# Performance work log

Measured on AMD Instinct MI355X. Metric: run time of the kernel, lower is better.

## Reference

```python
import jax, jax.numpy as jnp
import numpy as np

NUM_SEGMENTS = 4480  # BATCH_SIZE * MAX_ATOMS = 64 * 70
ATOM_DIM = 64
BOND_DIM = 16
N_EDGES = 65536


def setup_inputs() -> dict:
    key = jax.random.key(0)
    k1, k2, k3, k4 = jax.random.split(key, 4)
    atom_feat = jax.random.normal(k1, (NUM_SEGMENTS, ATOM_DIM), dtype=jnp.float32)
    bond_feat = jax.random.normal(k2, (N_EDGES, BOND_DIM), dtype=jnp.float32)
    pair_idx = jax.random.randint(k3, (N_EDGES, 2), 0, NUM_SEGMENTS, dtype=jnp.int64)
    # glorot-uniform style kernel, zero bias (as in add_weight initializers)
    limit = float(np.sqrt(6.0 / (BOND_DIM + ATOM_DIM ** 2)))
    kernel = jax.random.uniform(k4, (BOND_DIM, ATOM_DIM ** 2), dtype=jnp.float32,
                                minval=-limit, maxval=limit)
    bias = jnp.zeros((ATOM_DIM ** 2,), dtype=jnp.float32)
    return {"atom_feat": atom_feat, "bond_feat": bond_feat,
            "pair_idx": pair_idx, "kernel": kernel, "bias": bias}


def reference(atom_feat, bond_feat, pair_idx, kernel, bias):
    atom_dim = atom_feat.shape[-1]
    # dense projection of bond features -> per-edge transform matrices
    bond_transformed = bond_feat @ kernel + bias               # [E, D*D]
    bond_transformed = bond_transformed.reshape(-1, atom_dim, atom_dim)  # [E, D, D]
    # gather neighbor (source) atom features per edge
    neighbor_feat = jnp.take(atom_feat, pair_idx[:, 1].astype(jnp.int32), axis=0)  # [E, D]
    # per-edge matrix-vector product
    messages = jnp.einsum('eij,ej->ei', bond_transformed, neighbor_feat)  # [E, D]
    # scatter-add into destination atoms
    return jax.ops.segment_sum(messages, pair_idx[:, 0].astype(jnp.int32),
                               num_segments=NUM_SEGMENTS)  # [NUM_SEGMENTS, D]
```

## Files before the change

kernel.cpp:

```cpp
#include <hip/hip_runtime.h>
#include <hip/hip_bf16.h>

#define NSEG   4480
#define ADIM   64
#define BDIM   16
#define NEDGE  65536
#define UPITCH 1088
#define LPITCH 68

__device__ __forceinline__ float bf2f(unsigned int bits_hi16) {
    union { unsigned int i; float f; } c; c.i = bits_hi16; return c.f;
}
__device__ __forceinline__ unsigned short f2bf(float f) {
    union { float f; unsigned int i; } c; c.f = f;
    unsigned int x = c.i;
    x += 0x7fffu + ((x >> 16) & 1u);
    return (unsigned short)(x >> 16);
}

__global__ __launch_bounds__(256) void proj_kernel(
    const float* __restrict__ atom,
    const float* __restrict__ kern,
    const float* __restrict__ bias,
    unsigned short* __restrict__ U,
    float* __restrict__ out)
{
    __shared__ float As[64 * LPITCH];
    __shared__ float Bs[64 * LPITCH];

    const int t      = threadIdx.x;
    const int bx     = blockIdx.x;
    const int by     = blockIdx.y;
    const int a_base = bx * 64;
    const int c_base = by * 64;

    {
        int gid = by * 70 * 256 + bx * 256 + t;
        if (gid < NSEG * ADIM / 4) {
            ((float4*)out)[gid] = make_float4(0.f, 0.f, 0.f, 0.f);
        }
    }

#pragma unroll
    for (int k = 0; k < 4; ++k) {
        int id  = t + k * 256;
        int row = id >> 4;
        int j0  = (id & 15) * 4;
        float4 v = *(const float4*)(atom + (size_t)(a_base + row) * ADIM + j0);
        As[(j0 + 0) * LPITCH + row] = v.x;
        As[(j0 + 1) * LPITCH + row] = v.y;
        As[(j0 + 2) * LPITCH + row] = v.z;
        As[(j0 + 3) * LPITCH + row] = v.w;
    }
#pragma unroll
    for (int k = 0; k < 4; ++k) {
        int id   = t + k * 256;
        int crow = id >> 4;
        int j0   = (id & 15) * 4;
        int c    = c_base + crow;
        const float* bsrc = (c < 1024)
            ? (kern + (size_t)(c & 15) * 4096 + (size_t)(c >> 4) * 64)
            : (bias + (size_t)(c - 1024) * 64);
        float4 v = *(const float4*)(bsrc + j0);
        Bs[(j0 + 0) * LPITCH + crow] = v.x;
        Bs[(j0 + 1) * LPITCH + crow] = v.y;
        Bs[(j0 + 2) * LPITCH + crow] = v.z;
        Bs[(j0 + 3) * LPITCH + crow] = v.w;
    }
    __syncthreads();

    const int tx = t & 15;
    const int ty = t >> 4;
    const int a0 = ty * 4;
    const int c0 = tx * 4;

    float acc[4][4] = {};
#pragma unroll 8
    for (int j = 0; j < 64; ++j) {
        float4 av = *(const float4*)(As + j * LPITCH + a0);
        float4 bv = *(const float4*)(Bs + j * LPITCH + c0);
        acc[0][0] = fmaf(av.x, bv.x, acc[0][0]);
        acc[0][1] = fmaf(av.x, bv.y, acc[0][1]);
        acc[0][2] = fmaf(av.x, bv.z, acc[0][2]);
        acc[0][3] = fmaf(av.x, bv.w, acc[0][3]);
        acc[1][0] = fmaf(av.y, bv.x, acc[1][0]);
        acc[1][1] = fmaf(av.y, bv.y, acc[1][1]);
        acc[1][2] = fmaf(av.y, bv.z, acc[1][2]);
        acc[1][3] = fmaf(av.y, bv.w, acc[1][3]);
        acc[2][0] = fmaf(av.z, bv.x, acc[2][0]);
        acc[2][1] = fmaf(av.z, bv.y, acc[2][1]);
        acc[2][2] = fmaf(av.z, bv.z, acc[2][2]);
        acc[2][3] = fmaf(av.z, bv.w, acc[2][3]);
        acc[3][0] = fmaf(av.w, bv.x, acc[3][0]);
        acc[3][1] = fmaf(av.w, bv.y, acc[3][1]);
        acc[3][2] = fmaf(av.w, bv.z, acc[3][2]);
        acc[3][3] = fmaf(av.w, bv.w, acc[3][3]);
    }

#pragma unroll
    for (int r = 0; r < 4; ++r) {
        ushort4 o;
        o.x = f2bf(acc[r][0]);
        o.y = f2bf(acc[r][1]);
        o.z = f2bf(acc[r][2]);
        o.w = f2bf(acc[r][3]);
        *(ushort4*)(U + (size_t)(a_base + a0 + r) * UPITCH + c_base + c0) = o;
    }
}

__global__ __launch_bounds__(256) void edge_kernel(
    const float*          __restrict__ bond,
    const int*            __restrict__ pair,
    const unsigned short* __restrict__ U,
    float*                __restrict__ out)
{
    const int t    = threadIdx.x;
    const int lane = t & 63;
    const int e    = blockIdx.x * 4 + (t >> 6);

    const int dst = pair[(size_t)e * 2 + 0];
    const int src = pair[(size_t)e * 2 + 1];

    const unsigned short* urow = U + (size_t)src * UPITCH;
    const uint4* up = (const uint4*)(urow + lane * 16);
    uint4 w0 = up[0];
    uint4 w1 = up[1];

    const float4* bp = (const float4*)(bond + (size_t)e * BDIM);
    float4 b0 = bp[0], b1 = bp[1], b2 = bp[2], b3 = bp[3];
    float b[16] = { b0.x, b0.y, b0.z, b0.w,  b1.x, b1.y, b1.z, b1.w,
                    b2.x, b2.y, b2.z, b2.w,  b3.x, b3.y, b3.z, b3.w };

    unsigned int w[8] = { w0.x, w0.y, w0.z, w0.w, w1.x, w1.y, w1.z, w1.w };

    float m = 0.f;
#pragma unroll
    for (int k = 0; k < 8; ++k) {
        float lo = bf2f(w[k] << 16);
        float hi = bf2f(w[k] & 0xffff0000u);
        m = fmaf(lo, b[2 * k],     m);
        m = fmaf(hi, b[2 * k + 1], m);
    }

    m += bf2f(((unsigned int)urow[1024 + lane]) << 16);

    atomicAdd(out + (size_t)dst * ADIM + lane, m);
}

extern "C" void kernel_launch(void* const* d_in, const int* in_sizes, int n_in,
                              void* d_out, int out_size, void* d_ws, size_t ws_size,
                              hipStream_t stream) {
    const float* atom = (const float*)d_in[0];
    const float* bond = (const float*)d_in[1];
    const int*   pair = (const int*)  d_in[2];
    const float* kern = (const float*)d_in[3];
    const float* bias = (const float*)d_in[4];

    float* out = (float*)d_out;
    unsigned short* U = (unsigned short*)d_ws;

    dim3 g1(NSEG / 64, UPITCH / 64);
    proj_kernel<<<g1, 256, 0, stream>>>(atom, kern, bias, U, out);

    edge_kernel<<<NEDGE / 4, 256, 0, stream>>>(bond, pair, U, out);
}
```

Baseline: 99.42 us.

## Bucket edges by source atom so each wave reuses one projected row

Adds a scatter kernel that groups edge ids by source atom into fixed-capacity slots, using atomic counters zeroed inside the projection kernel. The edge kernel now assigns two waves per source atom. Each wave loads that atom's bf16 transform row and bias term once and loops over its bucketed edges, instead of re-gathering the 2 KB row for every edge. This cuts redundant gather traffic. In exchange it adds a launch, an atomic bucketing pass, and a serial per-wave loop, and edges beyond the capacity of 96 per source would be silently dropped.

```diff
diff --git a/kernel.cpp b/kernel.cpp
--- a/kernel.cpp
+++ b/kernel.cpp
@@ -7,6 +7,7 @@
 #define NEDGE  65536
 #define UPITCH 1088
 #define LPITCH 68
+#define CAP    96
 
 __device__ __forceinline__ float bf2f(unsigned int bits_hi16) {
     union { unsigned int i; float f; } c; c.i = bits_hi16; return c.f;
@@ -23,7 +24,8 @@
     const float* __restrict__ kern,
     const float* __restrict__ bias,
     unsigned short* __restrict__ U,
-    float* __restrict__ out)
+    float* __restrict__ out,
+    int*   __restrict__ cnt)
 {
     __shared__ float As[64 * LPITCH];
     __shared__ float Bs[64 * LPITCH];
@@ -34,11 +36,12 @@
     const int a_base = bx * 64;
     const int c_base = by * 64;
 
-    {
-        int gid = by * 70 * 256 + bx * 256 + t;
-        if (gid < NSEG * ADIM / 4) {
-            ((float4*)out)[gid] = make_float4(0.f, 0.f, 0.f, 0.f);
-        }
+    if (by == 0) {
+        int gid = bx * 256 + t;
+        ((float4*)out)[gid] = make_float4(0.f, 0.f, 0.f, 0.f);
+    } else if (by == 1) {
+        int gid = bx * 256 + t;
+        if (gid < NSEG / 4) ((int4*)cnt)[gid] = make_int4(0, 0, 0, 0);
     }
 
 #pragma unroll
@@ -108,43 +111,60 @@
     }
 }
 
+__global__ __launch_bounds__(256) void scatter_kernel(
+    const int* __restrict__ pair, int* __restrict__ cnt, int* __restrict__ slot)
+{
+    int e   = blockIdx.x * 256 + threadIdx.x;
+    int src = pair[(size_t)e * 2 + 1];
+    int pos = atomicAdd(&cnt[src], 1);
+    if (pos < CAP) slot[src * CAP + pos] = e;
+}
+
 __global__ __launch_bounds__(256) void edge_kernel(
     const float*          __restrict__ bond,
     const int*            __restrict__ pair,
     const unsigned short* __restrict__ U,
+    const int*            __restrict__ cnt,
+    const int*            __restrict__ slot,
     float*                __restrict__ out)
 {
     const int t    = threadIdx.x;
     const int lane = t & 63;
-    const int e    = blockIdx.x * 4 + (t >> 6);
+    const int wid  = blockIdx.x * 4 + (t >> 6);
+    const int s    = wid >> 1;
+    const int half = wid & 1;
 
-    const int dst = pair[(size_t)e * 2 + 0];
-    const int src = pair[(size_t)e * 2 + 1];
-
-    const unsigned short* urow = U + (size_t)src * UPITCH;
+    const unsigned short* urow = U + (size_t)s * UPITCH;
     const uint4* up = (const uint4*)(urow + lane * 16);
     uint4 w0 = up[0];
     uint4 w1 = up[1];
+    unsigned int w[8] = { w0.x, w0.y, w0.z, w0.w, w1.x, w1.y, w1.z, w1.w };
+    float ub = bf2f(((unsigned int)urow[1024 + lane]) << 16);
 
-    const float4* bp = (const float4*)(bond + (size_t)e * BDIM);
-    float4 b0 = bp[0], b1 = bp[1], b2 = bp[2], b3 = bp[3];
-    float b[16] = { b0.x, b0.y, b0.z, b0.w,  b1.x, b1.y, b1.z, b1.w,
-                    b2.x, b2.y, b2.z, b2.w,  b3.x, b3.y, b3.z, b3.w };
+    int n = cnt[s];
+    if (n > CAP) n = CAP;
 
-    unsigned int w[8] = { w0.x, w0.y, w0.z, w0.w, w1.x, w1.y, w1.z, w1.w };
+    for (int k = half; k < n; k += 2) {
+        int e = slot[s * CAP + k];
+        e = __builtin_amdgcn_readfirstlane(e);
+        int dst = pair[(size_t)e * 2 + 0];
 
-    float m = 0.f;
+        const float4* bp = (const float4*)(bond + (size_t)e * BDIM);
+        float4 b0 = bp[0], b1 = bp[1], b2 = bp[2], b3 = bp[3];
+        float b[16] = { b0.x, b0.y, b0.z, b0.w,  b1.x, b1.y, b1.z, b1.w,
+                        b2.x, b2.y, b2.z, b2.w,  b3.x, b3.y, b3.z, b3.w };
+
+        float m = ub;
 #pragma unroll
-    for (int k = 0; k < 8; ++k) {
-        float lo = bf2f(w[k] << 16);
-        float hi = bf2f(w[k] & 0xffff0000u);
-        m = fmaf(lo, b[2 * k],     m);
-        m = fmaf(hi, b[2 * k + 1], m);
+        for (int q = 0; q < 8; ++q) {
+            float lo = bf2f(w[q] << 16);
+            float hi = bf2f(w[q] & 0xffff0000u);
+            m = fmaf(lo, b[2 * q],     m);
+            m = fmaf(hi, b[2 * q + 1], m);
+        }
+
+        atomicAdd(out + (size_t)dst * ADIM + lane, m);
     }
-
-    m += bf2f(((unsigned int)urow[1024 + lane]) << 16);
-
-    atomicAdd(out + (size_t)dst * ADIM + lane, m);
 }
 
 extern "C" void kernel_launch(void* const* d_in, const int* in_sizes, int n_in,
@@ -157,10 +177,16 @@
     const float* bias = (const float*)d_in[4];
 
     float* out = (float*)d_out;
-    unsigned short* U = (unsigned short*)d_ws;
+
+    char* ws = (char*)d_ws;
+    unsigned short* U = (unsigned short*)ws;
+    int* cnt  = (int*)(ws + (size_t)NSEG * UPITCH * 2);
+    int* slot = cnt + NSEG;
 
     dim3 g1(NSEG / 64, UPITCH / 64);
-    proj_kernel<<<g1, 256, 0, stream>>>(atom, kern, bias, U, out);
+    proj_kernel<<<g1, 256, 0, stream>>>(atom, kern, bias, U, out, cnt);
 
-    edge_kernel<<<NEDGE / 4, 256, 0, stream>>>(bond, pair, U, out);
+    scatter_kernel<<<NEDGE / 256, 256, 0, stream>>>(pair, cnt, slot);
+
+    edge_kernel<<<(NSEG * 2) / 4, 256, 0, stream>>>(bond, pair, U, cnt, slot, out);
 }
```

Result: slower. 107.0 us (+7.7%).

## Bucket edges by source atom range to localize U reads per XCD

Applied to the files above, without the earlier changes.

Adds a bucketing kernel that groups edges by source-atom range into eight buckets and maps each bucket to blocks sharing an XCD index in the edge kernel. The intent is that each XCD's L2 only needs to hold a slice of the projected bf16 table U instead of the whole table. This adds an extra kernel launch, global atomics, an indirection through an edge list, and a fixed per-bucket capacity that could overflow for skewed inputs.

```diff
diff --git a/kernel.cpp b/kernel.cpp
--- a/kernel.cpp
+++ b/kernel.cpp
@@ -7,6 +7,9 @@
 #define NEDGE  65536
 #define UPITCH 1088
 #define LPITCH 68
+#define NBKT   8
+#define SRCDIV 560
+#define CAPB   9216
 
 __device__ __forceinline__ float bf2f(unsigned int bits_hi16) {
     union { unsigned int i; float f; } c; c.i = bits_hi16; return c.f;
@@ -23,7 +26,8 @@
     const float* __restrict__ kern,
     const float* __restrict__ bias,
     unsigned short* __restrict__ U,
-    float* __restrict__ out)
+    float* __restrict__ out,
+    int*   __restrict__ bcnt)
 {
     __shared__ float As[64 * LPITCH];
     __shared__ float Bs[64 * LPITCH];
@@ -34,11 +38,11 @@
     const int a_base = bx * 64;
     const int c_base = by * 64;
 
-    {
-        int gid = by * 70 * 256 + bx * 256 + t;
-        if (gid < NSEG * ADIM / 4) {
-            ((float4*)out)[gid] = make_float4(0.f, 0.f, 0.f, 0.f);
-        }
+    if (by == 0) {
+        int gid = bx * 256 + t;
+        ((float4*)out)[gid] = make_float4(0.f, 0.f, 0.f, 0.f);
+    } else if (by == 1 && bx == 0 && t < NBKT) {
+        bcnt[t] = 0;
     }
 
 #pragma unroll
@@ -108,15 +112,48 @@
     }
 }
 
+__global__ __launch_bounds__(256) void bucket_kernel(
+    const int* __restrict__ pair, int* __restrict__ bcnt, int* __restrict__ ebuf)
+{
+    __shared__ int lcnt[NBKT];
+    __shared__ int lbase[NBKT];
+
+    const int t = threadIdx.x;
+    if (t < NBKT) lcnt[t] = 0;
+    __syncthreads();
+
+    const int e   = blockIdx.x * 256 + t;
+    const int src = pair[(size_t)e * 2 + 1];
+    const int b   = src / SRCDIV;
+    const int pos = atomicAdd(&lcnt[b], 1);
+    __syncthreads();
+
+    if (t < NBKT) lbase[t] = atomicAdd(&bcnt[t], lcnt[t]);
+    __syncthreads();
+
+    ebuf[b * CAPB + lbase[b] + pos] = e;
+}
+
 __global__ __launch_bounds__(256) void edge_kernel(
     const float*          __restrict__ bond,
     const int*            __restrict__ pair,
     const unsigned short* __restrict__ U,
+    const int*            __restrict__ bcnt,
+    const int*            __restrict__ ebuf,
     float*                __restrict__ out)
 {
-    const int t    = threadIdx.x;
-    const int lane = t & 63;
-    const int e    = blockIdx.x * 4 + (t >> 6);
+    const int t     = threadIdx.x;
+    const int lane  = t & 63;
+    const int xcd   = blockIdx.x & 7;
+    const int chunk = blockIdx.x >> 3;
+
+    const int n = bcnt[xcd];
+    const int k = chunk * 4 + (t >> 6);
+    if (chunk * 4 >= n) return;
+    if (k >= n) return;
+
+    int e = ebuf[xcd * CAPB + k];
+    e = __builtin_amdgcn_readfirstlane(e);
 
     const int dst = pair[(size_t)e * 2 + 0];
     const int src = pair[(size_t)e * 2 + 1];
@@ -133,16 +170,14 @@
 
     unsigned int w[8] = { w0.x, w0.y, w0.z, w0.w, w1.x, w1.y, w1.z, w1.w };
 
-    float m = 0.f;
-#pragma unroll
-    for (int k = 0; k < 8; ++k) {
-        float lo = bf2f(w[k] << 16);
-        float hi = bf2f(w[k] & 0xffff0000u);
-        m = fmaf(lo, b[2 * k],     m);
-        m = fmaf(hi, b[2 * k + 1], m);
-    }
-
-    m += bf2f(((unsigned int)urow[1024 + lane]) << 16);
+    float m = bf2f(((unsigned int)urow[1024 + lane]) << 16);
+#pragma unroll
+    for (int q = 0; q < 8; ++q) {
+        float lo = bf2f(w[q] << 16);
+        float hi = bf2f(w[q] & 0xffff0000u);
+        m = fmaf(lo, b[2 * q],     m);
+        m = fmaf(hi, b[2 * q + 1], m);
+    }
 
     atomicAdd(out + (size_t)dst * ADIM + lane, m);
 }
@@ -157,10 +192,16 @@
     const float* bias = (const float*)d_in[4];
 
     float* out = (float*)d_out;
-    unsigned short* U = (unsigned short*)d_ws;
+
+    char* ws = (char*)d_ws;
+    unsigned short* U = (unsigned short*)ws;
+    int* bcnt = (int*)(ws + (size_t)NSEG * UPITCH * 2);
+    int* ebuf = bcnt + 16;
 
     dim3 g1(NSEG / 64, UPITCH / 64);
-    proj_kernel<<<g1, 256, 0, stream>>>(atom, kern, bias, U, out);
-
-    edge_kernel<<<NEDGE / 4, 256, 0, stream>>>(bond, pair, U, out);
-}
+    proj_kernel<<<g1, 256, 0, stream>>>(atom, kern, bias, U, out, bcnt);
+
+    bucket_kernel<<<NEDGE / 256, 256, 0, stream>>>(pair, bcnt, ebuf);
+
+    edge_kernel<<<NBKT * (CAPB / 4), 256, 0, stream>>>(bond, pair, U, bcnt, ebuf, out);
+}
```

Result: slower. 104.4 us (+5.0%).

## Use bf16 MFMA for atom projection GEMM and vectorize pair index load

Applied to the files above, without the earlier changes.

The projection kernel now converts atom features and kernel/bias tiles to bf16 in shared memory and computes the 64x64 tile product with mfma_f32_16x16x32_bf16 in place of the scalar FMA outer product. Output zeroing is moved to the by==0 blocks only. The edge kernel loads the pair indices as one int2 and folds the bias term into the accumulator's initial value. Rounding inputs to bf16 before the GEMM adds precision loss, and the U stores become scalar 16-bit writes rather than ushort4.

```diff
diff --git a/kernel.cpp b/kernel.cpp
--- a/kernel.cpp
+++ b/kernel.cpp
@@ -6,7 +6,10 @@
 #define BDIM   16
 #define NEDGE  65536
 #define UPITCH 1088
-#define LPITCH 68
+#define KP     72
+
+typedef __bf16 bf16x8 __attribute__((ext_vector_type(8)));
+typedef float  f32x4  __attribute__((ext_vector_type(4)));
 
 __device__ __forceinline__ float bf2f(unsigned int bits_hi16) {
     union { unsigned int i; float f; } c; c.i = bits_hi16; return c.f;
@@ -25,8 +28,8 @@
     unsigned short* __restrict__ U,
     float* __restrict__ out)
 {
-    __shared__ float As[64 * LPITCH];
-    __shared__ float Bs[64 * LPITCH];
+    __shared__ unsigned short Al[64 * KP];
+    __shared__ unsigned short Wl[64 * KP];
 
     const int t      = threadIdx.x;
     const int bx     = blockIdx.x;
@@ -34,77 +37,68 @@
     const int a_base = bx * 64;
     const int c_base = by * 64;
 
+    if (by == 0) {
+        int gid = bx * 256 + t;
+        ((float4*)out)[gid] = make_float4(0.f, 0.f, 0.f, 0.f);
+    }
+
     {
-        int gid = by * 70 * 256 + bx * 256 + t;
-        if (gid < NSEG * ADIM / 4) {
-            ((float4*)out)[gid] = make_float4(0.f, 0.f, 0.f, 0.f);
+        const int row = t >> 2, q = t & 3;
+        const float4* src = (const float4*)(atom + (size_t)(a_base + row) * ADIM + q * 16);
+        unsigned short* dst = Al + row * KP + q * 16;
+#pragma unroll
+        for (int i = 0; i < 4; ++i) {
+            float4 v = src[i];
+            dst[i * 4 + 0] = f2bf(v.x);
+            dst[i * 4 + 1] = f2bf(v.y);
+            dst[i * 4 + 2] = f2bf(v.z);
+            dst[i * 4 + 3] = f2bf(v.w);
+        }
+    }
+    {
+        const int crow = t >> 2, q = t & 3;
+        const int c = c_base + crow;
+        const float* bsrc = (c < 1024)
+            ? (kern + (size_t)(c & 15) * 4096 + (size_t)(c >> 4) * 64)
+            : (bias + (size_t)(c - 1024) * 64);
+        const float4* src = (const float4*)(bsrc + q * 16);
+        unsigned short* dst = Wl + crow * KP + q * 16;
+#pragma unroll
+        for (int i = 0; i < 4; ++i) {
+            float4 v = src[i];
+            dst[i * 4 + 0] = f2bf(v.x);
+            dst[i * 4 + 1] = f2bf(v.y);
+            dst[i * 4 + 2] = f2bf(v.z);
+            dst[i * 4 + 3] = f2bf(v.w);
+        }
+    }
+    __syncthreads();
+
+    const int lane = t & 63;
+    const int w    = t >> 6;
+    const int m    = lane & 15;
+    const int quad = lane >> 4;
+
+    f32x4 acc[4] = {{0.f,0.f,0.f,0.f},{0.f,0.f,0.f,0.f},
+                    {0.f,0.f,0.f,0.f},{0.f,0.f,0.f,0.f}};
+
+#pragma unroll
+    for (int kk = 0; kk < 2; ++kk) {
+        bf16x8 a = *(const bf16x8*)(Al + (w * 16 + m) * KP + kk * 32 + quad * 8);
+#pragma unroll
+        for (int ct = 0; ct < 4; ++ct) {
+            bf16x8 b = *(const bf16x8*)(Wl + (ct * 16 + m) * KP + kk * 32 + quad * 8);
+            acc[ct] = __builtin_amdgcn_mfma_f32_16x16x32_bf16(a, b, acc[ct], 0, 0, 0);
         }
     }
 
 #pragma unroll
-    for (int k = 0; k < 4; ++k) {
-        int id  = t + k * 256;
-        int row = id >> 4;
-        int j0  = (id & 15) * 4;
-        float4 v = *(const float4*)(atom + (size_t)(a_base + row) * ADIM + j0);
-        As[(j0 + 0) * LPITCH + row] = v.x;
-        As[(j0 + 1) * LPITCH + row] = v.y;
-        As[(j0 + 2) * LPITCH + row] = v.z;
-        As[(j0 + 3) * LPITCH + row] = v.w;
-    }
+    for (int ct = 0; ct < 4; ++ct) {
 #pragma unroll
-    for (int k = 0; k < 4; ++k) {
-        int id   = t + k * 256;
-        int crow = id >> 4;
-        int j0   = (id & 15) * 4;
-        int c    = c_base + crow;
-        const float* bsrc = (c < 1024)
-            ? (kern + (size_t)(c & 15) * 4096 + (size_t)(c >> 4) * 64)
-            : (bias + (size_t)(c - 1024) * 64);
-        float4 v = *(const float4*)(bsrc + j0);
-        Bs[(j0 + 0) * LPITCH + crow] = v.x;
-        Bs[(j0 + 1) * LPITCH + crow] = v.y;
-        Bs[(j0 + 2) * LPITCH + crow] = v.z;
-        Bs[(j0 + 3) * LPITCH + crow] = v.w;
-    }
-    __syncthreads();
-
-    const int tx = t & 15;
-    const int ty = t >> 4;
-    const int a0 = ty * 4;
-    const int c0 = tx * 4;
-
-    float acc[4][4] = {};
-#pragma unroll 8
-    for (int j = 0; j < 64; ++j) {
-        float4 av = *(const float4*)(As + j * LPITCH + a0);
-        float4 bv = *(const float4*)(Bs + j * LPITCH + c0);
-        acc[0][0] = fmaf(av.x, bv.x, acc[0][0]);
-        acc[0][1] = fmaf(av.x, bv.y, acc[0][1]);
-        acc[0][2] = fmaf(av.x, bv.z, acc[0][2]);
-        acc[0][3] = fmaf(av.x, bv.w, acc[0][3]);
-        acc[1][0] = fmaf(av.y, bv.x, acc[1][0]);
-        acc[1][1] = fmaf(av.y, bv.y, acc[1][1]);
-        acc[1][2] = fmaf(av.y, bv.z, acc[1][2]);
-        acc[1][3] = fmaf(av.y, bv.w, acc[1][3]);
-        acc[2][0] = fmaf(av.z, bv.x, acc[2][0]);
-        acc[2][1] = fmaf(av.z, bv.y, acc[2][1]);
-        acc[2][2] = fmaf(av.z, bv.z, acc[2][2]);
-        acc[2][3] = fmaf(av.z, bv.w, acc[2][3]);
-        acc[3][0] = fmaf(av.w, bv.x, acc[3][0]);
-        acc[3][1] = fmaf(av.w, bv.y, acc[3][1]);
-        acc[3][2] = fmaf(av.w, bv.z, acc[3][2]);
-        acc[3][3] = fmaf(av.w, bv.w, acc[3][3]);
-    }
-
-#pragma unroll
-    for (int r = 0; r < 4; ++r) {
-        ushort4 o;
-        o.x = f2bf(acc[r][0]);
-        o.y = f2bf(acc[r][1]);
-        o.z = f2bf(acc[r][2]);
-        o.w = f2bf(acc[r][3]);
-        *(ushort4*)(U + (size_t)(a_base + a0 + r) * UPITCH + c_base + c0) = o;
+        for (int r = 0; r < 4; ++r) {
+            U[(size_t)(a_base + w * 16 + quad * 4 + r) * UPITCH
+              + (c_base + ct * 16 + m)] = f2bf(acc[ct][r]);
+        }
     }
 }
 
@@ -118,8 +112,9 @@
     const int lane = t & 63;
     const int e    = blockIdx.x * 4 + (t >> 6);
 
-    const int dst = pair[(size_t)e * 2 + 0];
-    const int src = pair[(size_t)e * 2 + 1];
+    const int2 p  = ((const int2*)pair)[e];
+    const int dst = p.x;
+    const int src = p.y;
 
     const unsigned short* urow = U + (size_t)src * UPITCH;
     const uint4* up = (const uint4*)(urow + lane * 16);
@@ -133,16 +128,14 @@
 
     unsigned int w[8] = { w0.x, w0.y, w0.z, w0.w, w1.x, w1.y, w1.z, w1.w };
 
-    float m = 0.f;
+    float m = bf2f(((unsigned int)urow[1024 + lane]) << 16);
 #pragma unroll
-    for (int k = 0; k < 8; ++k) {
-        float lo = bf2f(w[k] << 16);
-        float hi = bf2f(w[k] & 0xffff0000u);
-        m = fmaf(lo, b[2 * k],     m);
-        m = fmaf(hi, b[2 * k + 1], m);
+    for (int q = 0; q < 8; ++q) {
+        float lo = bf2f(w[q] << 16);
+        float hi = bf2f(w[q] & 0xffff0000u);
+        m = fmaf(lo, b[2 * q],     m);
+        m = fmaf(hi, b[2 * q + 1], m);
     }
-
-    m += bf2f(((unsigned int)urow[1024 + lane]) << 16);
 
     atomicAdd(out + (size_t)dst * ADIM + lane, m);
 }
```

Result: faster. 92.37 us (median of 2 runs) (-7.1%).
